# Performance work log

Hardware: AMD Instinct MI355X
Metric: run time of the kernel (lower is better)

Reference implementation:

```python
import jax, jax.numpy as jnp
import numpy as np

TAU = 100.0
DT = 20.0
ALPHA = DT / TAU  # 0.2, fixed buffer (train_alpha=False)


def setup_inputs() -> dict:
    key = jax.random.key(0)
    ks = jax.random.split(key, 12)
    T, B, I, H = 64, 32, 128, 256

    def lin(kw, out_f, in_f):
        bound = 1.0 / np.sqrt(in_f)
        kw1, kw2 = jax.random.split(kw)
        w = jax.random.uniform(kw1, (out_f, in_f), jnp.float32, -bound, bound)
        b = jax.random.uniform(kw2, (out_f,), jnp.float32, -bound, bound)
        return w, b

    w_i2h, b_i2h = lin(ks[0], H, I)
    w_h2h, b_h2h = lin(ks[1], H, H)
    w_i2c, b_i2c = lin(ks[2], H, I)
    w_c2c, b_c2c = lin(ks[3], H, H)
    w_c2t, b_c2t = lin(ks[4], H * H, H)
    x = jax.random.normal(ks[5], (T, B, I), jnp.float32)
    return {
        "input": x,
        "w_i2h": w_i2h, "b_i2h": b_i2h,
        "w_h2h": w_h2h, "b_h2h": b_h2h,
        "w_i2c": w_i2c, "b_i2c": b_i2c,
        "w_c2c": w_c2c, "b_c2c": b_c2c,
        "w_c2t": w_c2t, "b_c2t": b_c2t,
        "num_steps": 1,
    }


def reference(input, w_i2h, b_i2h, w_h2h, b_h2h, w_i2c, b_i2c,
              w_c2c, b_c2c, w_c2t, b_c2t, num_steps):
    H = w_i2h.shape[0]
    B = input.shape[1]
    a = jnp.float32(ALPHA)

    def recurrence(x, hidden, context):
        input_proj = x @ w_i2h.T + b_i2h                      # [B,H]
        tm = (context @ w_c2t.T + b_c2t).reshape(B, H, H)     # per-sample hypernet matrix
        transformed = jnp.einsum('bij,bj->bi', tm, input_proj)
        h_new = jax.nn.relu(context + transformed + hidden @ w_h2h.T + b_h2h)
        hidden = hidden * (1 - a) + h_new * a
        context_new = jax.nn.relu(context @ w_c2c.T + b_c2c + x @ w_i2c.T + b_i2c)
        context = context * (1 - a) + context_new * a
        hidden = transformed  # NOTE: faithful to source, overwrites leaky update
        return hidden, context

    def step(carry, x):
        hidden, context = carry
        for _ in range(num_steps):
            hidden, context = recurrence(x, hidden, context)
        return (hidden, context), hidden

    h0 = jnp.zeros((B, H), input.dtype)
    c0 = jnp.zeros((B, H), input.dtype)
    (hidden, context), output = jax.lax.scan(step, (h0, c0), input)
    return output, hidden, context
```

## Files before the change

### kernel.cpp

```cpp
#include <hip/hip_runtime.h>

#define TT 64
#define BB 32
#define II 128
#define HH 256
#define MM (TT*BB)

typedef __bf16  bf16x8  __attribute__((ext_vector_type(8)));
typedef float   f32x16  __attribute__((ext_vector_type(16)));
typedef _Float16 half2v __attribute__((ext_vector_type(2)));
typedef unsigned int u32;

__device__ __forceinline__ float bf2f(unsigned short u) {
    union { unsigned int i; float f; } v; v.i = ((unsigned int)u) << 16; return v.f;
}
__device__ __forceinline__ unsigned short f2bf(float f) {
    union { float f; unsigned int i; } v; v.f = f;
    unsigned int r = v.i + 0x7fffu + ((v.i >> 16) & 1u);
    return (unsigned short)(r >> 16);
}

__device__ __forceinline__ void gload16(const unsigned short* g, unsigned short* l) {
    __builtin_amdgcn_global_load_lds(
        (const __attribute__((address_space(1))) u32*)g,
        (__attribute__((address_space(3))) u32*)l,
        16, 0, 0);
}

struct F8 { float v[8]; };
__device__ __forceinline__ F8 load8(const void* base, int idx, int isf32) {
    F8 r;
    if (isf32) {
        const float4* p = (const float4*)((const float*)base + idx);
        float4 a = p[0], b = p[1];
        r.v[0]=a.x; r.v[1]=a.y; r.v[2]=a.z; r.v[3]=a.w;
        r.v[4]=b.x; r.v[5]=b.y; r.v[6]=b.z; r.v[7]=b.w;
    } else {
        uint4 u = *(const uint4*)((const unsigned short*)base + idx);
        const unsigned short* p = (const unsigned short*)&u;
#pragma unroll
        for (int j = 0; j < 8; ++j) r.v[j] = bf2f(p[j]);
    }
    return r;
}
__device__ __forceinline__ float load1(const void* base, int idx, int isf32) {
    return isf32 ? ((const float*)base)[idx]
                 : bf2f(((const unsigned short*)base)[idx]);
}

__device__ __forceinline__ float fdot2f(half2v a, half2v b, float c) {
#if __has_builtin(__builtin_amdgcn_fdot2)
    return __builtin_amdgcn_fdot2(a, b, c, false);
#else
    return c + (float)a.x*(float)b.x + (float)a.y*(float)b.y;
#endif
}

__global__ __launch_bounds__(256) void k0_sniff(
    const unsigned short* __restrict__ x, int* __restrict__ flag)
{
    __shared__ int cnt;
    if (threadIdx.x == 0) cnt = 0;
    __syncthreads();
    int c = 0;
    for (int i = threadIdx.x; i < 8192; i += 256) {
        unsigned int e = (x[i] >> 7) & 0xFFu;
        if (e >= 0xC0u) ++c;
    }
    atomicAdd(&cnt, c);
    __syncthreads();
    if (threadIdx.x == 0) flag[0] = (cnt > 16) ? 1 : 0;
}

__global__ __launch_bounds__(256) void k1_proj(
    const void* __restrict__ x,
    const void* __restrict__ w_i2h,
    const void* __restrict__ b_i2h,
    const void* __restrict__ w_i2c,
    const void* __restrict__ b_i2c,
    const int* __restrict__ flagp,
    unsigned short* __restrict__ ipT,
    float* __restrict__ cin)
{
    const int isf32 = *flagp;
    const int tid = threadIdx.x;
    const int h = tid;
    const int mbase = blockIdx.x * 32;
    __shared__ __align__(16) _Float16 xs[32][II];
    __shared__ __align__(16) unsigned short ips[32][HH];

    half2v w1[II/2], w2[II/2];
#pragma unroll
    for (int c8 = 0; c8 < II/8; ++c8) {
        F8 f1 = load8(w_i2h, h*II + c8*8, isf32);
        F8 f2 = load8(w_i2c, h*II + c8*8, isf32);
#pragma unroll
        for (int j = 0; j < 4; ++j) {
            half2v a; a.x = (_Float16)f1.v[2*j]; a.y = (_Float16)f1.v[2*j+1];
            half2v b; b.x = (_Float16)f2.v[2*j]; b.y = (_Float16)f2.v[2*j+1];
            w1[c8*4 + j] = a;
            w2[c8*4 + j] = b;
        }
    }
    const float bb1 = load1(b_i2h, h, isf32);
    const float bb2 = load1(b_i2c, h, isf32);

    for (int u = tid; u < 32*II; u += 256)
        xs[u >> 7][u & (II-1)] = (_Float16)load1(x, (mbase + (u >> 7))*II + (u & (II-1)), isf32);
    __syncthreads();

    for (int mm = 0; mm < 32; ++mm) {
        const half2v* xv = (const half2v*)xs[mm];
        float a0=0,a1=0,a2=0,a3=0, c0=0,c1=0,c2=0,c3=0;
#pragma unroll
        for (int r = 0; r < II/2; r += 4) {
            half2v x0 = xv[r], x1 = xv[r+1], x2 = xv[r+2], x3 = xv[r+3];
            a0 = fdot2f(w1[r],   x0, a0);
            a1 = fdot2f(w1[r+1], x1, a1);
            a2 = fdot2f(w1[r+2], x2, a2);
            a3 = fdot2f(w1[r+3], x3, a3);
            c0 = fdot2f(w2[r],   x0, c0);
            c1 = fdot2f(w2[r+1], x1, c1);
            c2 = fdot2f(w2[r+2], x2, c2);
            c3 = fdot2f(w2[r+3], x3, c3);
        }
        ips[mm][h] = f2bf(((a0+a1)+(a2+a3)) + bb1);
        cin[(mbase+mm)*HH + h] = ((c0+c1)+(c2+c3)) + bb2;
    }
    __syncthreads();
    unsigned short tmp[32];
#pragma unroll
    for (int mm = 0; mm < 32; ++mm) tmp[mm] = ips[mm][tid];
    uint4* dst = (uint4*)(ipT + (size_t)tid*MM + mbase);
    const uint4* s4 = (const uint4*)tmp;
    dst[0] = s4[0]; dst[1] = s4[1]; dst[2] = s4[2]; dst[3] = s4[3];
}

__global__ __launch_bounds__(256) void k2_ctx(
    const void* __restrict__ w_c2c,
    const void* __restrict__ b_c2c,
    const float* __restrict__ cin,
    const int* __restrict__ ns_ptr,
    const int* __restrict__ flagp,
    unsigned short* __restrict__ ctx_hist,
    void* __restrict__ out_base)
{
    const int isf32 = *flagp;
    const int b = blockIdx.x;
    const int h = threadIdx.x;
    const int ns = max(1, *ns_ptr);

    __shared__ __align__(16) _Float16 cs[2][HH];

    half2v w[HH/2];
#pragma unroll
    for (int c8 = 0; c8 < HH/8; ++c8) {
        F8 f = load8(w_c2c, h*HH + c8*8, isf32);
#pragma unroll
        for (int j = 0; j < 4; ++j) {
            half2v hv;
            hv.x = (_Float16)f.v[2*j];
            hv.y = (_Float16)f.v[2*j+1];
            w[c8*4 + j] = hv;
        }
    }
    const float bcc = load1(b_c2c, h, isf32);
    float ctxv = 0.0f;
    cs[0][h] = (_Float16)0.0f;
    __syncthreads();
    int cur = 0;

    for (int t = 0; t < TT; ++t) {
        const float cinv = cin[(t*BB + b)*HH + h];
        for (int s = 0; s < ns; ++s) {
            if (s == ns-1) ctx_hist[(t*BB + b)*HH + h] = f2bf(ctxv);
            float p0=0,p1=0,p2=0,p3=0;
            const float4* cp4 = (const float4*)cs[cur];
#pragma unroll
            for (int r4 = 0; r4 < HH/8; ++r4) {
                float4 blob = cp4[r4];
                const half2v* c2 = (const half2v*)&blob;
                p0 = fdot2f(w[r4*4+0], c2[0], p0);
                p1 = fdot2f(w[r4*4+1], c2[1], p1);
                p2 = fdot2f(w[r4*4+2], c2[2], p2);
                p3 = fdot2f(w[r4*4+3], c2[3], p3);
            }
            float cnew = fmaxf(((p0+p1)+(p2+p3)) + bcc + cinv, 0.0f);
            ctxv = 0.8f*ctxv + 0.2f*cnew;
            cs[cur^1][h] = (_Float16)ctxv;
            cur ^= 1;
            __syncthreads();
        }
    }
    const int cofs = MM*HH + BB*HH + b*HH + h;
    if (isf32) ((float*)out_base)[cofs] = ctxv;
    else       ((unsigned short*)out_base)[cofs] = f2bf(ctxv);
}

__global__ __launch_bounds__(256) void k25_zero(float* __restrict__ outT)
{
    const int idx = (blockIdx.x * 256 + threadIdx.x) * 4;
    *(float4*)(outT + idx) = make_float4(0.f, 0.f, 0.f, 0.f);
}

__global__ __launch_bounds__(512, 4) void k3_main(
    const unsigned short* __restrict__ ctx_hist,
    const void* __restrict__ wc,
    const void* __restrict__ bc,
    const unsigned short* __restrict__ ipT,
    const int* __restrict__ flagp,
    float* __restrict__ outT)
{
    extern __shared__ __align__(16) unsigned char lds[];
    unsigned short* Ws  = (unsigned short*)lds;
    unsigned short* As0 = (unsigned short*)(lds + 65536);
    unsigned short* As1 = (unsigned short*)(lds + 73728);
    float*          Ps  = (float*)(lds + 65536);

    const int isf32 = *flagp;
    const int tid  = threadIdx.x;
    const int lane = tid & 63;
    const int wave = tid >> 6;
    const int bx   = blockIdx.x;
    const int i    = bx >> 1;
    const int jh   = bx & 1;
    const int jq   = wave & 1;
    const int ms   = wave >> 1;
    const int l31  = lane & 31;
    const int lhi  = lane >> 5;

#pragma unroll
    for (int p = 0; p < 8; ++p) {
        const int u = tid + p*512;
        const int jrow = u >> 5, cu = u & 31;
        F8 f = load8(wc, (i*HH + jh*128 + jrow)*HH + cu*8, isf32);
        unsigned short tmp[8];
#pragma unroll
        for (int j = 0; j < 8; ++j) tmp[j] = f2bf(f.v[j]);
        *(uint4*)(Ws + (cu*128 + jrow)*8) = *(const uint4*)tmp;
    }

    const int trow = tid & 255;
    const int tku  = tid >> 8;
    const int wbofs = (tid & ~63) * 8;
    unsigned short* wAs0 = As0 + wbofs;
    unsigned short* wAs1 = As1 + wbofs;

    const unsigned short* wfA = Ws + (jq*64 + l31)*8;
    const unsigned short* wfB = Ws + (jq*64 + 32 + l31)*8;
    const int abase = (lhi*256 + ms*64 + l31)*8;

    gload16(ctx_hist + trow*HH + tku*8, wAs0);

#pragma unroll 1
    for (int mc = 0; mc < 8; ++mc) {
        const unsigned short* gsrc = ctx_hist + (mc*256 + trow)*HH + tku*8;

        f32x16 acc[2][2];
#pragma unroll
        for (int a = 0; a < 2; ++a)
#pragma unroll
            for (int g = 0; g < 4; ++g) {
                const int jb = i*HH + jh*128 + jq*64 + a*32 + g*8 + lhi*4;
                float b0, b1, b2, b3;
                if (isf32) {
                    float4 t = *(const float4*)((const float*)bc + jb);
                    b0 = t.x; b1 = t.y; b2 = t.z; b3 = t.w;
                } else {
                    ushort4 t = *(const ushort4*)((const unsigned short*)bc + jb);
                    b0 = bf2f(t.x); b1 = bf2f(t.y); b2 = bf2f(t.z); b3 = bf2f(t.w);
                }
                acc[a][0][g*4+0] = b0; acc[a][1][g*4+0] = b0;
                acc[a][0][g*4+1] = b1; acc[a][1][g*4+1] = b1;
                acc[a][0][g*4+2] = b2; acc[a][1][g*4+2] = b2;
                acc[a][0][g*4+3] = b3; acc[a][1][g*4+3] = b3;
            }

#pragma unroll
        for (int kc = 0; kc < 16; ++kc) {
            __syncthreads();
            if (kc < 15)
                gload16(gsrc + (kc+1)*16, (kc & 1) ? wAs0 : wAs1);
            const unsigned short* Ac = (kc & 1) ? As1 : As0;
            const int uA = kc*2 + lhi;
            bf16x8 w0 = *(const bf16x8*)(wfA + uA*1024);
            bf16x8 w1 = *(const bf16x8*)(wfB + uA*1024);
            bf16x8 b0 = *(const bf16x8*)(Ac + abase);
            bf16x8 b1 = *(const bf16x8*)(Ac + abase + 32*8);
            __builtin_amdgcn_s_setprio(1);
            acc[0][0] = __builtin_amdgcn_mfma_f32_32x32x16_bf16(w0, b0, acc[0][0], 0, 0, 0);
            acc[0][1] = __builtin_amdgcn_mfma_f32_32x32x16_bf16(w0, b1, acc[0][1], 0, 0, 0);
            acc[1][0] = __builtin_amdgcn_mfma_f32_32x32x16_bf16(w1, b0, acc[1][0], 0, 0, 0);
            acc[1][1] = __builtin_amdgcn_mfma_f32_32x32x16_bf16(w1, b1, acc[1][1], 0, 0, 0);
            __builtin_amdgcn_s_setprio(0);
        }

        float sv0 = 0.0f, sv1 = 0.0f;
        const int mcol = mc*256 + ms*64 + l31;
#pragma unroll
        for (int a = 0; a < 2; ++a)
#pragma unroll
            for (int g = 0; g < 4; ++g) {
                const unsigned short* prow =
                    ipT + (jh*128 + jq*64 + a*32 + g*8 + lhi*4)*MM + mcol;
#pragma unroll
                for (int q = 0; q < 4; ++q) {
                    sv0 = fmaf(acc[a][0][g*4+q], bf2f(prow[q*MM]),      sv0);
                    sv1 = fmaf(acc[a][1][g*4+q], bf2f(prow[q*MM + 32]), sv1);
                }
            }
        sv0 += __shfl_xor(sv0, 32);
        sv1 += __shfl_xor(sv1, 32);
        if (lhi == 0) {
            Ps[jq*256 + ms*64 +      l31] = sv0;
            Ps[jq*256 + ms*64 + 32 + l31] = sv1;
        }
        __syncthreads();
        if (tid < 256)
            atomicAdd(&outT[(size_t)i*MM + mc*256 + tid], Ps[tid] + Ps[256+tid]);
        __syncthreads();
        if (mc < 7)
            gload16(ctx_hist + ((mc+1)*256 + trow)*HH + tku*8, wAs0);
    }
}

__global__ __launch_bounds__(256) void k4_tr(
    const float* __restrict__ outT,
    const int* __restrict__ flagp,
    void* __restrict__ out)
{
    const int isf32 = *flagp;
    __shared__ float tile[64][65];
    const int t  = threadIdx.x;
    const int bm = blockIdx.x * 64;
    const int bi = blockIdx.y * 64;
#pragma unroll
    for (int p = 0; p < 16; ++p) {
        const int u = t + p*256;
        const int r = u >> 6, c = u & 63;
        tile[r][c] = outT[(size_t)(bi + r)*MM + bm + c];
    }
    __syncthreads();
#pragma unroll
    for (int p = 0; p < 16; ++p) {
        const int u = t + p*256;
        const int r = u >> 6, c = u & 63;
        const float v = tile[c][r];
        const int m = bm + r;
        if (isf32) {
            float* o = (float*)out;
            o[(size_t)m*HH + bi + c] = v;
            if (m >= MM - BB) o[(size_t)MM*HH + (m - (MM-BB))*HH + bi + c] = v;
        } else {
            unsigned short* o = (unsigned short*)out;
            const unsigned short vb = f2bf(v);
            o[(size_t)m*HH + bi + c] = vb;
            if (m >= MM - BB) o[(size_t)MM*HH + (m - (MM-BB))*HH + bi + c] = vb;
        }
    }
}

extern "C" void kernel_launch(void* const* d_in, const int* in_sizes, int n_in,
                              void* d_out, int out_size, void* d_ws, size_t ws_size,
                              hipStream_t stream) {
    const void* x     = d_in[0];
    const void* w_i2h = d_in[1];
    const void* b_i2h = d_in[2];
    const void* w_i2c = d_in[5];
    const void* b_i2c = d_in[6];
    const void* w_c2c = d_in[7];
    const void* b_c2c = d_in[8];
    const void* w_c2t = d_in[9];
    const void* b_c2t = d_in[10];
    const int* ns     = (const int*)d_in[11];

    unsigned short* ipT = (unsigned short*)d_ws;
    unsigned short* ch  = (unsigned short*)((char*)d_ws + (size_t)MM*HH*2);
    float* cin          = (float*)((char*)d_ws + (size_t)MM*HH*4);
    float* outT         = cin;
    int* flag           = (int*)((char*)d_ws + (size_t)MM*HH*8);

    (void)hipFuncSetAttribute((const void*)k3_main,
                              hipFuncAttributeMaxDynamicSharedMemorySize, 81920);

    k0_sniff<<<1, 256, 0, stream>>>((const unsigned short*)x, flag);
    k1_proj<<<64, 256, 0, stream>>>(x, w_i2h, b_i2h, w_i2c, b_i2c, flag, ipT, cin);
    k2_ctx<<<BB, 256, 0, stream>>>(w_c2c, b_c2c, cin, ns, flag, ch, d_out);
    k25_zero<<<512, 256, 0, stream>>>(outT);
    k3_main<<<512, 512, 81920, stream>>>(ch, w_c2t, b_c2t, ipT, flag, outT);
    k4_tr<<<dim3(32, 4), 256, 0, stream>>>(outT, flag, d_out);
}
```

Measured before the change: 368.0 us.

## Replace double-buffered A tiles with 4-slot LDS ring and vmcnt waits

The k3_main GEMM loop moves from a 2-buffer, 16-step K pipeline with a full __syncthreads per step to a 4-slot LDS ring of 32-wide K chunks. Loads are issued three chunks ahead and each step waits with explicit s_waitcnt vmcnt before a bare barrier. Dynamic LDS grows from 80KB to 128KB and launch bounds drop to 2 blocks/CU. The aim is fewer barriers and deeper prefetch to hide global latency, at the cost of lower occupancy.

```diff
diff --git a/kernel.cpp b/kernel.cpp
--- a/kernel.cpp
+++ b/kernel.cpp
@@ -203,7 +203,7 @@
     *(float4*)(outT + idx) = make_float4(0.f, 0.f, 0.f, 0.f);
 }
 
-__global__ __launch_bounds__(512, 4) void k3_main(
+__global__ __launch_bounds__(512, 2) void k3_main(
     const unsigned short* __restrict__ ctx_hist,
     const void* __restrict__ wc,
     const void* __restrict__ bc,
@@ -212,10 +212,9 @@
     float* __restrict__ outT)
 {
     extern __shared__ __align__(16) unsigned char lds[];
-    unsigned short* Ws  = (unsigned short*)lds;
-    unsigned short* As0 = (unsigned short*)(lds + 65536);
-    unsigned short* As1 = (unsigned short*)(lds + 73728);
-    float*          Ps  = (float*)(lds + 65536);
+    unsigned short* Ws   = (unsigned short*)lds;
+    unsigned short* ring = (unsigned short*)(lds + 65536);
+    float*          Ps   = (float*)(lds + 65536);
 
     const int isf32 = *flagp;
     const int tid  = threadIdx.x;
@@ -239,22 +238,21 @@
         for (int j = 0; j < 8; ++j) tmp[j] = f2bf(f.v[j]);
         *(uint4*)(Ws + (cu*128 + jrow)*8) = *(const uint4*)tmp;
     }
-
-    const int trow = tid & 255;
-    const int tku  = tid >> 8;
-    const int wbofs = (tid & ~63) * 8;
-    unsigned short* wAs0 = As0 + wbofs;
-    unsigned short* wAs1 = As1 + wbofs;
-
-    const unsigned short* wfA = Ws + (jq*64 + l31)*8;
-    const unsigned short* wfB = Ws + (jq*64 + 32 + l31)*8;
-    const int abase = (lhi*256 + ms*64 + l31)*8;
-
-    gload16(ctx_hist + trow*HH + tku*8, wAs0);
+    asm volatile("s_waitcnt lgkmcnt(0)" ::: "memory");
+
+    const int u0 = wave*128 + lane;
+    const int m0row = u0 & 255, k0u = u0 >> 8;
+    const int u1 = u0 + 64;
+    const int m1row = u1 & 255, k1u = u1 >> 8;
+    const int wb0 = (wave*128)*8;
+    const int wb1 = (wave*128 + 64)*8;
+
+    const int wbase = (jq*64 + l31)*8;
+    const int bofs  = (lhi*256 + ms*64 + l31)*8;
 
 #pragma unroll 1
     for (int mc = 0; mc < 8; ++mc) {
-        const unsigned short* gsrc = ctx_hist + (mc*256 + trow)*HH + tku*8;
+        const unsigned short* gm = ctx_hist + (size_t)(mc*256)*HH;
 
         f32x16 acc[2][2];
 #pragma unroll
@@ -277,22 +275,37 @@
             }
 
 #pragma unroll
-        for (int kc = 0; kc < 16; ++kc) {
-            __syncthreads();
-            if (kc < 15)
-                gload16(gsrc + (kc+1)*16, (kc & 1) ? wAs0 : wAs1);
-            const unsigned short* Ac = (kc & 1) ? As1 : As0;
-            const int uA = kc*2 + lhi;
-            bf16x8 w0 = *(const bf16x8*)(wfA + uA*1024);
-            bf16x8 w1 = *(const bf16x8*)(wfB + uA*1024);
-            bf16x8 b0 = *(const bf16x8*)(Ac + abase);
-            bf16x8 b1 = *(const bf16x8*)(Ac + abase + 32*8);
-            __builtin_amdgcn_s_setprio(1);
-            acc[0][0] = __builtin_amdgcn_mfma_f32_32x32x16_bf16(w0, b0, acc[0][0], 0, 0, 0);
-            acc[0][1] = __builtin_amdgcn_mfma_f32_32x32x16_bf16(w0, b1, acc[0][1], 0, 0, 0);
-            acc[1][0] = __builtin_amdgcn_mfma_f32_32x32x16_bf16(w1, b0, acc[1][0], 0, 0, 0);
-            acc[1][1] = __builtin_amdgcn_mfma_f32_32x32x16_bf16(w1, b1, acc[1][1], 0, 0, 0);
-            __builtin_amdgcn_s_setprio(0);
+        for (int c = 0; c < 3; ++c) {
+            gload16(gm + m0row*HH + c*32 + k0u*8, ring + c*8192 + wb0);
+            gload16(gm + m1row*HH + c*32 + k1u*8, ring + c*8192 + wb1);
+        }
+
+#pragma unroll
+        for (int kc = 0; kc < 8; ++kc) {
+            if (kc < 6)       asm volatile("s_waitcnt vmcnt(4)" ::: "memory");
+            else if (kc == 6) asm volatile("s_waitcnt vmcnt(2)" ::: "memory");
+            else              asm volatile("s_waitcnt vmcnt(0)" ::: "memory");
+            __builtin_amdgcn_s_barrier();
+            if (kc < 5) {
+                const int c = kc + 3, rb = c & 3;
+                gload16(gm + m0row*HH + c*32 + k0u*8, ring + rb*8192 + wb0);
+                gload16(gm + m1row*HH + c*32 + k1u*8, ring + rb*8192 + wb1);
+            }
+            const unsigned short* Ac = ring + (kc & 3)*8192;
+#pragma unroll
+            for (int ks = 0; ks < 2; ++ks) {
+                const int ku = kc*4 + ks*2 + lhi;
+                bf16x8 w0 = *(const bf16x8*)(Ws + ku*1024 + wbase);
+                bf16x8 w1 = *(const bf16x8*)(Ws + ku*1024 + wbase + 256);
+                bf16x8 b0 = *(const bf16x8*)(Ac + bofs + ks*4096);
+                bf16x8 b1 = *(const bf16x8*)(Ac + bofs + ks*4096 + 256);
+                __builtin_amdgcn_s_setprio(1);
+                acc[0][0] = __builtin_amdgcn_mfma_f32_32x32x16_bf16(w0, b0, acc[0][0], 0, 0, 0);
+                acc[0][1] = __builtin_amdgcn_mfma_f32_32x32x16_bf16(w0, b1, acc[0][1], 0, 0, 0);
+                acc[1][0] = __builtin_amdgcn_mfma_f32_32x32x16_bf16(w1, b0, acc[1][0], 0, 0, 0);
+                acc[1][1] = __builtin_amdgcn_mfma_f32_32x32x16_bf16(w1, b1, acc[1][1], 0, 0, 0);
+                __builtin_amdgcn_s_setprio(0);
+            }
         }
 
         float sv0 = 0.0f, sv1 = 0.0f;
@@ -319,8 +332,6 @@
         if (tid < 256)
             atomicAdd(&outT[(size_t)i*MM + mc*256 + tid], Ps[tid] + Ps[256+tid]);
         __syncthreads();
-        if (mc < 7)
-            gload16(ctx_hist + ((mc+1)*256 + trow)*HH + tku*8, wAs0);
     }
 }
 
@@ -381,12 +392,12 @@
     int* flag           = (int*)((char*)d_ws + (size_t)MM*HH*8);
 
     (void)hipFuncSetAttribute((const void*)k3_main,
-                              hipFuncAttributeMaxDynamicSharedMemorySize, 81920);
+                              hipFuncAttributeMaxDynamicSharedMemorySize, 131072);
 
     k0_sniff<<<1, 256, 0, stream>>>((const unsigned short*)x, flag);
     k1_proj<<<64, 256, 0, stream>>>(x, w_i2h, b_i2h, w_i2c, b_i2c, flag, ipT, cin);
     k2_ctx<<<BB, 256, 0, stream>>>(w_c2c, b_c2c, cin, ns, flag, ch, d_out);
     k25_zero<<<512, 256, 0, stream>>>(outT);
-    k3_main<<<512, 512, 81920, stream>>>(ch, w_c2t, b_c2t, ipT, flag, outT);
+    k3_main<<<512, 512, 131072, stream>>>(ch, w_c2t, b_c2t, ipT, flag, outT);
     k4_tr<<<dim3(32, 4), 256, 0, stream>>>(outT, flag, d_out);
 }
```

Result: faster. 332.4 us (-9.7%).
